# Kernel optimization log

Measured on AMD Instinct MI355X. Metric: run time of the kernel, lower is better.

## Reference

```python
import jax, jax.numpy as jnp
import numpy as np
from jax import lax

NUM_POINTS = 1024  # num_points from __init__
BIG = jnp.float32(1e10)


def setup_inputs() -> dict:
    key = jax.random.key(0)
    B, N = 8, 131072
    points = jax.random.normal(key, (B, N, 3), dtype=jnp.float32)
    return {"points": points}


def furthest_point_sampling(points, m):
    """points: [B, N, 3] -> indices [B, m] (int32).
    Standard FPS: start at index 0, iteratively pick the point farthest
    from the current selected set, maintaining a running min-distance.
    """
    B, N, _ = points.shape

    def body(carry, _):
        min_dist, last_idx = carry  # [B, N], [B]
        last_pt = jnp.take_along_axis(points, last_idx[:, None, None], axis=1)  # [B,1,3]
        d = jnp.sum((points - last_pt) ** 2, axis=-1)  # [B, N]
        min_dist = jnp.minimum(min_dist, d)
        nxt = jnp.argmax(min_dist, axis=-1).astype(jnp.int32)  # [B]
        return (min_dist, nxt), nxt

    init_idx = jnp.zeros((B,), dtype=jnp.int32)
    init_dist = jnp.full((B, N), BIG, dtype=points.dtype)
    _, rest = lax.scan(body, (init_dist, init_idx), None, length=m - 1)  # [m-1, B]
    idx = jnp.concatenate([init_idx[None, :], rest], axis=0)  # [m, B]
    return idx.T  # [B, m]


def reference(points):
    idx = furthest_point_sampling(points, NUM_POINTS)            # [B, m]
    xyz1 = jnp.take_along_axis(points, idx[:, :, None], axis=1)  # [B, m, 3]
    return (idx, xyz1)
```

## Files before the change

### kernel.cpp

```cpp
#include <hip/hip_runtime.h>
#include <stdint.h>


#define BATCHES 8
#define NPTS    131072
#define MSEL    1024
#define NBLK    32
#define CHUNK   (NPTS / NBLK)
#define NTH     256
#define PPT     (CHUNK / NTH)
#define NWAVE   (NTH / 64)
#define L2_TIMEOUT_ROUNDS 2000

__device__ __forceinline__ unsigned long long l2_load_u64(
    const unsigned long long* p) {
    unsigned long long v;
    asm volatile("global_load_dwordx2 %0, %1, off sc0\n\t"
                 "s_waitcnt vmcnt(0)"
                 : "=v"(v) : "v"(p) : "memory");
    return v;
}
__device__ __forceinline__ void l2_store_u64(unsigned long long* p,
                                             unsigned long long v) {
    asm volatile("global_store_dwordx2 %0, %1, off sc0"
                 :: "v"(p), "v"(v) : "memory");
}

__global__ __launch_bounds__(NTH, 1) void fps_kernel(
    const float* __restrict__ pts,
    float* __restrict__ out,
    unsigned long long* __restrict__ l2slots,
    unsigned long long* __restrict__ icslots)
{
    __shared__ unsigned long long wkey[NWAVE];
    __shared__ float curs[4];

    const int bid   = blockIdx.x;
    const int b     = bid & (BATCHES - 1);
    const int blk   = bid / BATCHES;
    const int tid   = threadIdx.x;
    const int gbase = blk * CHUNK;
    const float* bp = pts + (size_t)b * NPTS * 3;

    float px[PPT], py[PPT], pz[PPT], md[PPT];
    #pragma unroll
    for (int k = 0; k < PPT; ++k) {
        const int j = gbase + k * NTH + tid;
        const size_t gi = (size_t)j * 3;
        px[k] = bp[gi + 0];
        py[k] = bp[gi + 1];
        pz[k] = bp[gi + 2];
        md[k] = 1e10f;
    }
    const unsigned int relt = (unsigned int)(NPTS - 1) - (unsigned int)(gbase + tid);

    float cx = bp[0], cy = bp[1], cz = bp[2];
    if (blk == 0 && tid == 0) {
        out[b * MSEL] = 0.0f;
        float* oxyz = out + BATCHES * MSEL;
        oxyz[(size_t)(b * MSEL) * 3 + 0] = cx;
        oxyz[(size_t)(b * MSEL) * 3 + 1] = cy;
        oxyz[(size_t)(b * MSEL) * 3 + 2] = cz;
    }

    const int wv = tid >> 6;
    const int ln = tid & 63;
    bool useAgent = false;

    for (int s = 1; s < MSEL; ++s) {
        unsigned long long bk = 0ull;
        #pragma unroll
        for (int k = 0; k < PPT; ++k) {
            float dx = __fsub_rn(px[k], cx);
            float dy = __fsub_rn(py[k], cy);
            float dz = __fsub_rn(pz[k], cz);
            float d  = __fadd_rn(__fadd_rn(__fmul_rn(dx, dx), __fmul_rn(dy, dy)),
                                 __fmul_rn(dz, dz));
            float nm = fminf(md[k], d);
            md[k] = nm;
            unsigned long long key =
                ((unsigned long long)__float_as_uint(nm) << 32)
                | (unsigned long long)(relt - (unsigned int)(k * NTH));
            bk = (bk > key) ? bk : key;
        }
        #pragma unroll
        for (int o = 32; o > 0; o >>= 1) {
            unsigned long long t = __shfl_xor(bk, o, 64);
            bk = (bk > t) ? bk : t;
        }
        if (ln == 0) wkey[wv] = bk;
        __syncthreads();

        const unsigned int tag = (unsigned int)s;
        const size_t slbase = ((size_t)(s & 1) * BATCHES + b) * NBLK;

        if (wv == 1 && ln == 0) {
            unsigned long long k0 = wkey[0];
            #pragma unroll
            for (int w = 1; w < NWAVE; ++w) k0 = (k0 > wkey[w]) ? k0 : wkey[w];
            const unsigned long long sv =
                ((k0 >> 32) << 27) | ((k0 & 0x1FFFFull) << 10) | tag;
            __hip_atomic_store(&icslots[slbase + blk], sv,
                               __ATOMIC_RELAXED, __HIP_MEMORY_SCOPE_AGENT);
        }

        if (wv == 0) {
            if (ln == 0) {
                unsigned long long k0 = wkey[0];
                #pragma unroll
                for (int w = 1; w < NWAVE; ++w) k0 = (k0 > wkey[w]) ? k0 : wkey[w];
                const unsigned long long sv =
                    ((k0 >> 32) << 27) | ((k0 & 0x1FFFFull) << 10) | tag;
                l2_store_u64(&l2slots[slbase + blk], sv);
            }
            unsigned long long k = 0ull;
            if (!useAgent) {
                int r = 0;
                for (;;) {
                    if (ln < NBLK) k = l2_load_u64(&l2slots[slbase + ln]);
                    if (__all((ln >= NBLK) | ((unsigned int)(k & 1023ull) == tag)))
                        break;
                    if (++r >= L2_TIMEOUT_ROUNDS) { useAgent = true; break; }
                    __builtin_amdgcn_s_sleep(1);
                }
            }
            if (useAgent) {
                for (;;) {
                    if (ln < NBLK)
                        k = __hip_atomic_load(&icslots[slbase + ln],
                                              __ATOMIC_RELAXED,
                                              __HIP_MEMORY_SCOPE_AGENT);
                    if (__all((ln >= NBLK) | ((unsigned int)(k & 1023ull) == tag)))
                        break;
                    __builtin_amdgcn_s_sleep(1);
                }
            }
            #pragma unroll
            for (int o = 16; o > 0; o >>= 1) {
                unsigned long long t = __shfl_xor(k, o, 64);
                k = (k > t) ? k : t;
            }
            const unsigned int widx =
                (unsigned int)(NPTS - 1) - (unsigned int)((k >> 10) & 0x1FFFFull);
            if (ln < 3) {
                const float v = bp[(size_t)widx * 3 + ln];
                curs[ln] = v;
                if (blk == 0)
                    out[BATCHES * MSEL + (size_t)(b * MSEL + s) * 3 + ln] = v;
            }
            if (ln == 0 && blk == 0) out[b * MSEL + s] = (float)widx;
        }
        __syncthreads();
        cx = curs[0]; cy = curs[1]; cz = curs[2];
    }
}

extern "C" void kernel_launch(void* const* d_in, const int* in_sizes, int n_in,
                              void* d_out, int out_size, void* d_ws, size_t ws_size,
                              hipStream_t stream) {
    const float* pts = (const float*)d_in[0];
    float* out = (float*)d_out;
    unsigned long long* l2slots = (unsigned long long*)d_ws;
    unsigned long long* icslots = (unsigned long long*)((char*)d_ws + 4096);

    fps_kernel<<<dim3(BATCHES * NBLK), dim3(NTH), 0, stream>>>(
        pts, out, l2slots, icslots);
}
```

Baseline: 2.332 ms.

## Publish winner coordinates in padded L2 slots to skip dependent global gather

Each block keeps its chunk's coordinates in LDS and writes its local winner's xyz into its L2 exchange slot together with the key and tag. Slots are padded to 128 bytes when workspace allows. The reading wave reduces key and coordinates together with shuffles, so the dependent global load of the winning point after the cross-block reduction goes away. In exchange, each slot write and read grows to two vector memory ops, 48 KB of LDS is used, and completion is checked with a duplicated tag per slot.

Measured after the change: 2.249 ms. 1.04x faster.

```diff
diff --git a/kernel.cpp b/kernel.cpp
--- a/kernel.cpp
+++ b/kernel.cpp
@@ -12,27 +12,39 @@
 #define NWAVE   (NTH / 64)
 #define L2_TIMEOUT_ROUNDS 2000
 
-__device__ __forceinline__ unsigned long long l2_load_u64(
-    const unsigned long long* p) {
-    unsigned long long v;
-    asm volatile("global_load_dwordx2 %0, %1, off sc0\n\t"
+typedef unsigned int       u32;
+typedef unsigned long long u64;
+typedef u32 u32x4 __attribute__((ext_vector_type(4)));
+typedef u32 u32x2 __attribute__((ext_vector_type(2)));
+
+__device__ __forceinline__ void l2_store_slot(void* p, u32x4 a, u32x2 b) {
+    asm volatile("global_store_dwordx4 %0, %1, off sc0\n\t"
+                 "global_store_dwordx2 %2, %3, off sc0"
+                 :: "v"((u32*)p), "v"(a), "v"(((u32*)p) + 4), "v"(b)
+                 : "memory");
+}
+__device__ __forceinline__ void l2_load_slot(const void* p, u32x4& a, u32x2& b) {
+    u32x4 ra; u32x2 rb;
+    asm volatile("global_load_dwordx4 %0, %2, off sc0\n\t"
+                 "global_load_dwordx2 %1, %3, off sc0\n\t"
                  "s_waitcnt vmcnt(0)"
-                 : "=v"(v) : "v"(p) : "memory");
-    return v;
-}
-__device__ __forceinline__ void l2_store_u64(unsigned long long* p,
-                                             unsigned long long v) {
-    asm volatile("global_store_dwordx2 %0, %1, off sc0"
-                 :: "v"(p), "v"(v) : "memory");
+                 : "=&v"(ra), "=&v"(rb)
+                 : "v"((const u32*)p), "v"(((const u32*)p) + 4)
+                 : "memory");
+    a = ra; b = rb;
 }
 
 __global__ __launch_bounds__(NTH, 1) void fps_kernel(
     const float* __restrict__ pts,
     float* __restrict__ out,
-    unsigned long long* __restrict__ l2slots,
-    unsigned long long* __restrict__ icslots)
+    char* __restrict__ l2base,
+    u64*  __restrict__ icslots,
+    int pad)
 {
-    __shared__ unsigned long long wkey[NWAVE];
+    __shared__ float lx[CHUNK];
+    __shared__ float ly[CHUNK];
+    __shared__ float lz[CHUNK];
+    __shared__ u64 wkey[NWAVE];
     __shared__ float curs[4];
 
     const int bid   = blockIdx.x;
@@ -45,14 +57,15 @@
     float px[PPT], py[PPT], pz[PPT], md[PPT];
     #pragma unroll
     for (int k = 0; k < PPT; ++k) {
-        const int j = gbase + k * NTH + tid;
-        const size_t gi = (size_t)j * 3;
+        const int j = k * NTH + tid;
+        const size_t gi = (size_t)(gbase + j) * 3;
         px[k] = bp[gi + 0];
         py[k] = bp[gi + 1];
         pz[k] = bp[gi + 2];
         md[k] = 1e10f;
+        lx[j] = px[k]; ly[j] = py[k]; lz[j] = pz[k];
     }
-    const unsigned int relt = (unsigned int)(NPTS - 1) - (unsigned int)(gbase + tid);
+    const u32 relt = (u32)(NPTS - 1) - (u32)(gbase + tid);
 
     float cx = bp[0], cy = bp[1], cz = bp[2];
     if (blk == 0 && tid == 0) {
@@ -62,13 +75,14 @@
         oxyz[(size_t)(b * MSEL) * 3 + 1] = cy;
         oxyz[(size_t)(b * MSEL) * 3 + 2] = cz;
     }
+    __syncthreads();
 
     const int wv = tid >> 6;
     const int ln = tid & 63;
     bool useAgent = false;
 
     for (int s = 1; s < MSEL; ++s) {
-        unsigned long long bk = 0ull;
+        u64 bk = 0ull;
         #pragma unroll
         for (int k = 0; k < PPT; ++k) {
             float dx = __fsub_rn(px[k], cx);
@@ -78,77 +92,114 @@
                                  __fmul_rn(dz, dz));
             float nm = fminf(md[k], d);
             md[k] = nm;
-            unsigned long long key =
-                ((unsigned long long)__float_as_uint(nm) << 32)
-                | (unsigned long long)(relt - (unsigned int)(k * NTH));
+            u64 key = ((u64)__float_as_uint(nm) << 17)
+                    | (u64)(relt - (u32)(k * NTH));
             bk = (bk > key) ? bk : key;
         }
         #pragma unroll
         for (int o = 32; o > 0; o >>= 1) {
-            unsigned long long t = __shfl_xor(bk, o, 64);
+            u64 t = __shfl_xor(bk, o, 64);
             bk = (bk > t) ? bk : t;
         }
         if (ln == 0) wkey[wv] = bk;
         __syncthreads();
 
-        const unsigned int tag = (unsigned int)s;
-        const size_t slbase = ((size_t)(s & 1) * BATCHES + b) * NBLK;
+        const u32 tag = (u32)s;
+        char* base = l2base + ((size_t)(s & 1) * BATCHES + b) * NBLK * (size_t)pad;
+        const size_t icb = ((size_t)(s & 1) * BATCHES + b) * NBLK;
 
         if (wv == 1 && ln == 0) {
-            unsigned long long k0 = wkey[0];
+            u64 k0 = wkey[0];
             #pragma unroll
             for (int w = 1; w < NWAVE; ++w) k0 = (k0 > wkey[w]) ? k0 : wkey[w];
-            const unsigned long long sv =
-                ((k0 >> 32) << 27) | ((k0 & 0x1FFFFull) << 10) | tag;
-            __hip_atomic_store(&icslots[slbase + blk], sv,
+            const u64 sv = ((k0 >> 17) << 27) | ((k0 & 0x1FFFFull) << 10) | tag;
+            __hip_atomic_store(&icslots[icb + blk], sv,
                                __ATOMIC_RELAXED, __HIP_MEMORY_SCOPE_AGENT);
         }
 
         if (wv == 0) {
             if (ln == 0) {
-                unsigned long long k0 = wkey[0];
+                u64 k0 = wkey[0];
                 #pragma unroll
                 for (int w = 1; w < NWAVE; ++w) k0 = (k0 > wkey[w]) ? k0 : wkey[w];
-                const unsigned long long sv =
-                    ((k0 >> 32) << 27) | ((k0 & 0x1FFFFull) << 10) | tag;
-                l2_store_u64(&l2slots[slbase + blk], sv);
+                const u32 rel = (u32)(k0 & 0x1FFFFull);
+                const u32 db  = (u32)(k0 >> 17);
+                const int j   = (int)((u32)(NPTS - 1) - rel) - gbase;
+                u32x4 a; u32x2 bg;
+                a.x = db; a.y = (rel << 10) | tag;
+                a.z = __float_as_uint(lx[j]); a.w = __float_as_uint(ly[j]);
+                bg.x = __float_as_uint(lz[j]); bg.y = tag;
+                l2_store_slot(base + (size_t)blk * pad, a, bg);
             }
-            unsigned long long k = 0ull;
+            u64 k = 0ull; float x = 0.f, y = 0.f, z = 0.f;
             if (!useAgent) {
+                u32x4 A; u32x2 Bv; bool done = false;
                 int r = 0;
                 for (;;) {
-                    if (ln < NBLK) k = l2_load_u64(&l2slots[slbase + ln]);
-                    if (__all((ln >= NBLK) | ((unsigned int)(k & 1023ull) == tag)))
-                        break;
+                    if (ln < NBLK && !done) {
+                        l2_load_slot(base + (size_t)ln * pad, A, Bv);
+                        done = ((A.y & 1023u) == tag) & (Bv.y == tag);
+                    }
+                    if (__all((ln >= NBLK) | done)) break;
                     if (++r >= L2_TIMEOUT_ROUNDS) { useAgent = true; break; }
                     __builtin_amdgcn_s_sleep(1);
                 }
+                if (!useAgent && ln < NBLK) {
+                    k = ((u64)A.x << 17) | (u64)(A.y >> 10);
+                    x = __uint_as_float(A.z);
+                    y = __uint_as_float(A.w);
+                    z = __uint_as_float(Bv.x);
+                }
             }
             if (useAgent) {
+                u64 ak = 0ull;
                 for (;;) {
                     if (ln < NBLK)
-                        k = __hip_atomic_load(&icslots[slbase + ln],
-                                              __ATOMIC_RELAXED,
-                                              __HIP_MEMORY_SCOPE_AGENT);
-                    if (__all((ln >= NBLK) | ((unsigned int)(k & 1023ull) == tag)))
+                        ak = __hip_atomic_load(&icslots[icb + ln],
+                                               __ATOMIC_RELAXED,
+                                               __HIP_MEMORY_SCOPE_AGENT);
+                    if (__all((ln >= NBLK) | ((u32)(ak & 1023ull) == tag)))
                         break;
                     __builtin_amdgcn_s_sleep(1);
                 }
+                #pragma unroll
+                for (int o = 16; o > 0; o >>= 1) {
+                    u64 t = __shfl_xor(ak, o, 64);
+                    ak = (ak > t) ? ak : t;
+                }
+                const u32 widx = (u32)(NPTS - 1) - (u32)((ak >> 10) & 0x1FFFFull);
+                if (ln < 3) {
+                    const float v = bp[(size_t)widx * 3 + ln];
+                    curs[ln] = v;
+                    if (blk == 0)
+                        out[BATCHES * MSEL + (size_t)(b * MSEL + s) * 3 + ln] = v;
+                }
+                if (ln == 0 && blk == 0) out[b * MSEL + s] = (float)widx;
+            } else {
+                #pragma unroll
+                for (int o = 16; o > 0; o >>= 1) {
+                    u64 kk = __shfl_xor(k, o, 64);
+                    float xx = __shfl_xor(x, o, 64);
+                    float yy = __shfl_xor(y, o, 64);
+                    float zz = __shfl_xor(z, o, 64);
+                    const bool p = kk > k;
+                    k = p ? kk : k;
+                    x = p ? xx : x;
+                    y = p ? yy : y;
+                    z = p ? zz : z;
+                }
+                if (ln == 0) {
+                    const u32 widx = (u32)(NPTS - 1) - (u32)(k & 0x1FFFFull);
+                    curs[0] = x; curs[1] = y; curs[2] = z;
+                    if (blk == 0) {
+                        out[b * MSEL + s] = (float)widx;
+                        float* oxyz = out + BATCHES * MSEL;
+                        oxyz[(size_t)(b * MSEL + s) * 3 + 0] = x;
+                        oxyz[(size_t)(b * MSEL + s) * 3 + 1] = y;
+                        oxyz[(size_t)(b * MSEL + s) * 3 + 2] = z;
+                    }
+                }
             }
-            #pragma unroll
-            for (int o = 16; o > 0; o >>= 1) {
-                unsigned long long t = __shfl_xor(k, o, 64);
-                k = (k > t) ? k : t;
-            }
-            const unsigned int widx =
-                (unsigned int)(NPTS - 1) - (unsigned int)((k >> 10) & 0x1FFFFull);
-            if (ln < 3) {
-                const float v = bp[(size_t)widx * 3 + ln];
-                curs[ln] = v;
-                if (blk == 0)
-                    out[BATCHES * MSEL + (size_t)(b * MSEL + s) * 3 + ln] = v;
-            }
-            if (ln == 0 && blk == 0) out[b * MSEL + s] = (float)widx;
         }
         __syncthreads();
         cx = curs[0]; cy = curs[1]; cz = curs[2];
@@ -160,9 +211,12 @@
                               hipStream_t stream) {
     const float* pts = (const float*)d_in[0];
     float* out = (float*)d_out;
-    unsigned long long* l2slots = (unsigned long long*)d_ws;
-    unsigned long long* icslots = (unsigned long long*)((char*)d_ws + 4096);
+
+    const int pad = (ws_size >= (size_t)(2 * BATCHES * NBLK * 128 + 4096))
+                        ? 128 : 32;
+    char* l2base = (char*)d_ws;
+    u64* icslots = (u64*)((char*)d_ws + (size_t)2 * BATCHES * NBLK * pad);
 
     fps_kernel<<<dim3(BATCHES * NBLK), dim3(NTH), 0, stream>>>(
-        pts, out, l2slots, icslots);
-}
+        pts, out, l2base, icslots, pad);
+}
```
